# Kernel optimization log

Hardware: AMD Instinct MI355X
Metric: run time of the kernel (lower is better)

The kernel has to match this reference:

```python
import jax, jax.numpy as jnp
import numpy as np

B, S, D = 2, 2048, 1024
H = 16
HD = D // H  # 64

def setup_inputs() -> dict:
    key = jax.random.key(0)
    k1, k2, k3 = jax.random.split(key, 3)
    scale = 0.02
    return {
        "x": jax.random.normal(k1, (B, S, D), dtype=jnp.float32),
        "w_qkv": jax.random.normal(k2, (D, 3 * D), dtype=jnp.float32) * scale,
        "b_qkv": jnp.zeros((3 * D,), dtype=jnp.float32),
        "w_proj": jax.random.normal(k3, (D, D), dtype=jnp.float32) * scale,
        "b_proj": jnp.zeros((D,), dtype=jnp.float32),
    }

def reference(x, w_qkv, b_qkv, w_proj, b_proj):
    batch, seq_len, _ = x.shape
    qkv = x @ w_qkv + b_qkv                      # [B,S,3D]
    qkv = qkv.reshape(batch, seq_len, 3, H, HD)
    qkv = jnp.transpose(qkv, (2, 0, 3, 1, 4))    # [3,B,H,S,HD]
    q, k, v = qkv[0], qkv[1], qkv[2]
    attn = jnp.einsum('bhqd,bhkd->bhqk', q, k) / jnp.sqrt(jnp.float32(HD))
    attn = jax.nn.softmax(attn, axis=-1)         # [B,H,S,S]
    out = jnp.einsum('bhqk,bhkd->bhqd', attn, v)
    out = jnp.transpose(out, (0, 2, 1, 3)).reshape(batch, seq_len, -1)
    return out @ w_proj + b_proj
```

## Files before the change

### kernel.cpp

```cpp
#include <hip/hip_runtime.h>
#include <math.h>

#define SS 2048
#define DD 1024
#define HH 16
#define NQKV 3072
#define MROWS 4096
#define KD 1024

typedef __attribute__((ext_vector_type(8))) short bf16x8;
typedef __attribute__((ext_vector_type(8))) unsigned short us8;
typedef __attribute__((ext_vector_type(4))) float f32x4;
typedef unsigned short u16;
typedef unsigned int u32;

#define SCALE_C 0.18033688011112042f

#define GLDS16(g, l) \
  __builtin_amdgcn_global_load_lds((const __attribute__((address_space(1))) u32*)(g), \
                                   (__attribute__((address_space(3))) u32*)(l), 16, 0, 0)

static __device__ __forceinline__ u16 f2bf(float f) {
  union { float f; u32 u; } v; v.f = f;
  u32 u = v.u;
  u += 0x7fffu + ((u >> 16) & 1u);
  return (u16)(u >> 16);
}
static __device__ __forceinline__ u32 pk2(float a, float b) {
  return (u32)f2bf(a) | ((u32)f2bf(b) << 16);
}
static __device__ __forceinline__ u32 pk2t(float a, float b) {
  union { float f; u32 u; } ua, ub; ua.f = a; ub.f = b;
  return __builtin_amdgcn_perm(ub.u, ua.u, 0x07060302u);
}

__global__ __launch_bounds__(256) void k_prep(const float* __restrict__ x,
                                              const float* __restrict__ w_qkv,
                                              const float* __restrict__ w_proj,
                                              u16* __restrict__ x_bf,
                                              u16* __restrict__ wqkvT,
                                              u16* __restrict__ wprojT) {
  __shared__ float t[64][65];
  int bx = blockIdx.x;
  int tid = threadIdx.x;
  if (bx < 2048) {
    int i = (bx * 256 + tid) * 8;
    float4 a = *(const float4*)(x + i);
    float4 b = *(const float4*)(x + i + 4);
    us8 o;
    o[0] = f2bf(a.x); o[1] = f2bf(a.y); o[2] = f2bf(a.z); o[3] = f2bf(a.w);
    o[4] = f2bf(b.x); o[5] = f2bf(b.y); o[6] = f2bf(b.z); o[7] = f2bf(b.w);
    *(us8*)(x_bf + i) = o;
    return;
  }
  const float* in; u16* out; int R = KD, C, tile;
  if (bx < 2048 + 768) { in = w_qkv; out = wqkvT; C = NQKV; tile = bx - 2048; }
  else                 { in = w_proj; out = wprojT; C = DD; tile = bx - 2816; }
  int tilesC = C >> 6;
  int tc = tile % tilesC, tr = tile / tilesC;
  int r0 = tr * 64, c0 = tc * 64;
  int lx = tid & 63, ly = tid >> 6;
#pragma unroll
  for (int i = 0; i < 16; i++) {
    int rr = ly + i * 4;
    t[rr][lx] = in[(size_t)(r0 + rr) * C + c0 + lx];
  }
  __syncthreads();
#pragma unroll
  for (int i = 0; i < 16; i++) {
    int cc = ly + i * 4;
    out[(size_t)(c0 + cc) * R + r0 + lx] = f2bf(t[lx][cc]);
  }
}

template <int MODE, int BM>
__global__ __launch_bounds__(256, 2) void k_gemm(const u16* __restrict__ A,
                                                 const u16* __restrict__ Bt,
                                                 const float* __restrict__ bias,
                                                 void* __restrict__ Cout,
                                                 u16* __restrict__ vt,
                                                 int M, int N, int K) {
  constexpr int MT = BM / 32;
  __shared__ alignas(16) u16 As[BM * 64];
  __shared__ alignas(16) u16 Bs[128 * 64];
  const int tid = threadIdx.x;
  const int w = tid >> 6, ln = tid & 63;
  const int wm = w >> 1, wn = w & 1;
  const int lm = ln & 15, quad = ln >> 4;
  const int m0 = blockIdx.y * BM, n0 = blockIdx.x * 128;
  const int lr = ln >> 3, cc = ln & 7;
  const int cg = cc ^ lr;

  f32x4 acc[MT][4];
#pragma unroll
  for (int i = 0; i < MT; i++)
#pragma unroll
    for (int j = 0; j < 4; j++) acc[i][j] = (f32x4){0.f, 0.f, 0.f, 0.f};

  const u16* gA = A  + (size_t)(m0 + lr) * K + cg * 8;
  const u16* gB = Bt + (size_t)(n0 + lr) * K + cg * 8;

  for (int k0 = 0; k0 < K; k0 += 64) {
#pragma unroll
    for (int ii = 0; ii < MT; ii++) {
      int i = w + 4 * ii;
      GLDS16(gA + (size_t)(8 * i) * K + k0, (char*)As + i * 1024);
    }
#pragma unroll
    for (int ii = 0; ii < 4; ii++) {
      int i = w + 4 * ii;
      GLDS16(gB + (size_t)(8 * i) * K + k0, (char*)Bs + i * 1024);
    }
    __syncthreads();
    bf16x8 af[MT][2], bfr[4][2];
#pragma unroll
    for (int t = 0; t < MT; t++)
#pragma unroll
      for (int kk = 0; kk < 2; kk++)
        af[t][kk] = *(const bf16x8*)((const char*)As + (wm * (MT * 16) + t * 16 + lm) * 128 +
                                     (((kk * 4 + quad) ^ (lm & 7)) * 16));
#pragma unroll
    for (int t = 0; t < 4; t++)
#pragma unroll
      for (int kk = 0; kk < 2; kk++)
        bfr[t][kk] = *(const bf16x8*)((const char*)Bs + (wn * 64 + t * 16 + lm) * 128 +
                                      (((kk * 4 + quad) ^ (lm & 7)) * 16));
#pragma unroll
    for (int kk = 0; kk < 2; kk++)
#pragma unroll
      for (int mt = 0; mt < MT; mt++)
#pragma unroll
        for (int nt = 0; nt < 4; nt++)
          acc[mt][nt] = __builtin_amdgcn_mfma_f32_16x16x32_bf16(af[mt][kk], bfr[nt][kk], acc[mt][nt], 0, 0, 0);
    __syncthreads();
  }

  float bv[4];
#pragma unroll
  for (int nt = 0; nt < 4; nt++) bv[nt] = bias[n0 + wn * 64 + nt * 16 + lm];

  if (MODE == 2 && n0 >= 2 * DD) {
    int b = m0 >> 11;
    int s0 = (m0 & 2047) + wm * 64;
#pragma unroll
    for (int mt = 0; mt < MT; mt++) {
      int s = s0 + mt * 16 + quad * 4;
#pragma unroll
      for (int nt = 0; nt < 4; nt++) {
        int n = n0 + wn * 64 + nt * 16 + lm;
        int bh = b * HH + ((n - 2 * DD) >> 6);
        int d = n & 63;
        uint2 v;
        v.x = pk2(acc[mt][nt][0] + bv[nt], acc[mt][nt][1] + bv[nt]);
        v.y = pk2(acc[mt][nt][2] + bv[nt], acc[mt][nt][3] + bv[nt]);
        *(uint2*)&vt[(size_t)(bh * 64 + d) * SS + s] = v;
      }
    }
    return;
  }

  const float qs = (MODE == 2 && n0 < DD) ? SCALE_C : 1.0f;
#pragma unroll
  for (int mt = 0; mt < MT; mt++) {
#pragma unroll
    for (int r = 0; r < 4; r++) {
      int row = m0 + wm * (MT * 16) + mt * 16 + quad * 4 + r;
#pragma unroll
      for (int nt = 0; nt < 4; nt++) {
        int col = n0 + wn * 64 + nt * 16 + lm;
        float v = (acc[mt][nt][r] + bv[nt]) * qs;
        if (MODE == 2) ((u16*)Cout)[(size_t)row * N + col] = f2bf(v);
        else           ((float*)Cout)[(size_t)row * N + col] = v;
      }
    }
  }
}

__global__ __launch_bounds__(256, 2) void k_attn(const u16* __restrict__ qkv,
                                                 const u16* __restrict__ vt,
                                                 u16* __restrict__ attn) {
  __shared__ alignas(16) u16 Ks[2][128 * 64];
  __shared__ alignas(16) u16 Vs[2][64 * 128];
  __shared__ alignas(16) u16 Ps[4 * 32 * 64];

  const int tid = threadIdx.x;
  const int w = tid >> 6, ln = tid & 63;
  const int lm = ln & 15, quad = ln >> 4;
  const int bx = blockIdx.x;
  const int bh = bx >> 4;
  const int q0 = (bx & 15) * 128;
  const int b = bh >> 4, h = bh & 15;
  const size_t qkv_b = (size_t)b * SS * NQKV;
  const int hcol = h * 64;

  const int lr = ln >> 3, cc = ln & 7;
  const int cg = cc ^ lr;
  const int vr = ln >> 4, c16 = ln & 15;

  bf16x8 qf[2][2];
#pragma unroll
  for (int qs2 = 0; qs2 < 2; qs2++)
#pragma unroll
    for (int kk = 0; kk < 2; kk++)
      qf[qs2][kk] = *(const bf16x8*)(qkv + qkv_b +
                     (size_t)(q0 + w * 32 + qs2 * 16 + lm) * NQKV + hcol + kk * 32 + quad * 8);

  f32x4 o[4][2];
  float l[2] = {0.f, 0.f};
#pragma unroll
  for (int t = 0; t < 4; t++) { o[t][0] = (f32x4){0, 0, 0, 0}; o[t][1] = (f32x4){0, 0, 0, 0}; }

  char* psw = (char*)Ps + w * 4096;

#pragma unroll
  for (int rr = 0; rr < 4; rr++) {
    int i = w + 4 * rr;
    GLDS16(qkv + qkv_b + (size_t)(8 * i + lr) * NQKV + DD + hcol + cg * 8, (char*)Ks[0] + i * 1024);
    int cgv = c16 ^ ((4 * i + vr) & 15);
    GLDS16(vt + (size_t)(bh * 64 + 4 * i + vr) * SS + cgv * 8,             (char*)Vs[0] + i * 1024);
  }

#pragma unroll 1
  for (int it = 0; it < SS / 128; it++) {
    __syncthreads();

    if (it + 1 < SS / 128) {
      int kv1 = (it + 1) * 128;
      char* kd = (char*)Ks[(it + 1) & 1];
      char* vd = (char*)Vs[(it + 1) & 1];
#pragma unroll
      for (int rr = 0; rr < 4; rr++) {
        int i = w + 4 * rr;
        GLDS16(qkv + qkv_b + (size_t)(kv1 + 8 * i + lr) * NQKV + DD + hcol + cg * 8, kd + i * 1024);
        int cgv = c16 ^ ((4 * i + vr) & 15);
        GLDS16(vt + (size_t)(bh * 64 + 4 * i + vr) * SS + kv1 + cgv * 8,             vd + i * 1024);
      }
    }

    const char* ksb = (const char*)Ks[it & 1];
    const char* vsb = (const char*)Vs[it & 1];

#pragma unroll
    for (int sub = 0; sub < 2; sub++) {
      f32x4 s[4][2];
#pragma unroll
      for (int t = 0; t < 4; t++) { s[t][0] = (f32x4){0, 0, 0, 0}; s[t][1] = (f32x4){0, 0, 0, 0}; }
#pragma unroll
      for (int kk = 0; kk < 2; kk++)
#pragma unroll
        for (int t = 0; t < 4; t++) {
          bf16x8 kf = *(const bf16x8*)(ksb + (sub * 64 + t * 16 + lm) * 128 +
                                       (((kk * 4 + quad) ^ (lm & 7)) * 16));
          s[t][0] = __builtin_amdgcn_mfma_f32_16x16x32_bf16(kf, qf[0][kk], s[t][0], 0, 0, 0);
          s[t][1] = __builtin_amdgcn_mfma_f32_16x16x32_bf16(kf, qf[1][kk], s[t][1], 0, 0, 0);
        }

      bf16x8 vf[2][4];
#pragma unroll
      for (int kk = 0; kk < 2; kk++)
#pragma unroll
        for (int t = 0; t < 4; t++)
          vf[kk][t] = *(const bf16x8*)(vsb + (t * 16 + lm) * 256 +
                                       (((sub * 8 + kk * 4 + quad) ^ lm) * 16));

#pragma unroll
      for (int qs2 = 0; qs2 < 2; qs2++) {
        float sum = 0.f;
        u32 pkv[4][2];
#pragma unroll
        for (int t = 0; t < 4; t++) {
          float p0 = __builtin_amdgcn_exp2f(s[t][qs2][0]);
          float p1 = __builtin_amdgcn_exp2f(s[t][qs2][1]);
          float p2 = __builtin_amdgcn_exp2f(s[t][qs2][2]);
          float p3 = __builtin_amdgcn_exp2f(s[t][qs2][3]);
          sum += (p0 + p1) + (p2 + p3);
          pkv[t][0] = pk2t(p0, p1);
          pkv[t][1] = pk2t(p2, p3);
        }
        sum += __shfl_xor(sum, 16);
        sum += __shfl_xor(sum, 32);
        l[qs2] += sum;
#pragma unroll
        for (int t = 0; t < 4; t++) {
          uint2 v; v.x = pkv[t][0]; v.y = pkv[t][1];
          *(uint2*)(psw + (qs2 * 16 + lm) * 128 +
                    (((2 * t + (quad >> 1)) ^ (lm & 7)) * 16) + (quad & 1) * 8) = v;
        }
      }

      bf16x8 pf[2][2];
#pragma unroll
      for (int qs2 = 0; qs2 < 2; qs2++)
#pragma unroll
        for (int kk = 0; kk < 2; kk++)
          pf[qs2][kk] = *(const bf16x8*)(psw + (qs2 * 16 + lm) * 128 +
                                         (((kk * 4 + quad) ^ (lm & 7)) * 16));
#pragma unroll
      for (int kk = 0; kk < 2; kk++)
#pragma unroll
        for (int t = 0; t < 4; t++) {
          o[t][0] = __builtin_amdgcn_mfma_f32_16x16x32_bf16(vf[kk][t], pf[0][kk], o[t][0], 0, 0, 0);
          o[t][1] = __builtin_amdgcn_mfma_f32_16x16x32_bf16(vf[kk][t], pf[1][kk], o[t][1], 0, 0, 0);
        }
    }
  }

#pragma unroll
  for (int qs2 = 0; qs2 < 2; qs2++) {
    float il = 1.0f / l[qs2];
    int row = b * SS + q0 + w * 32 + qs2 * 16 + lm;
#pragma unroll
    for (int t = 0; t < 4; t++) {
      uint2 v;
      v.x = pk2(o[t][qs2][0] * il, o[t][qs2][1] * il);
      v.y = pk2(o[t][qs2][2] * il, o[t][qs2][3] * il);
      *(uint2*)&attn[(size_t)row * DD + hcol + t * 16 + quad * 4] = v;
    }
  }
}

extern "C" void kernel_launch(void* const* d_in, const int* in_sizes, int n_in,
                              void* d_out, int out_size, void* d_ws, size_t ws_size,
                              hipStream_t stream) {
  const float* x      = (const float*)d_in[0];
  const float* w_qkv  = (const float*)d_in[1];
  const float* b_qkv  = (const float*)d_in[2];
  const float* w_proj = (const float*)d_in[3];
  const float* b_proj = (const float*)d_in[4];
  float* out = (float*)d_out;

  u16* ws     = (u16*)d_ws;
  u16* x_bf   = ws;
  u16* wqkvT  = x_bf   + (size_t)MROWS * KD;
  u16* wprojT = wqkvT  + (size_t)NQKV * KD;
  u16* qkv    = wprojT + (size_t)DD * KD;
  u16* attn   = qkv    + (size_t)MROWS * NQKV;
  u16* vt     = attn   + (size_t)MROWS * DD;

  k_prep<<<3072, 256, 0, stream>>>(x, w_qkv, w_proj, x_bf, wqkvT, wprojT);
  k_gemm<2, 128><<<dim3(NQKV / 128, MROWS / 128), 256, 0, stream>>>(x_bf, wqkvT, b_qkv, qkv, vt, MROWS, NQKV, KD);
  k_attn<<<2 * HH * (SS / 128), 256, 0, stream>>>(qkv, vt, attn);
  k_gemm<0, 64><<<dim3(DD / 128, MROWS / 64), 256, 0, stream>>>(attn, wprojT, b_proj, out, nullptr, MROWS, DD, KD);
}
```

Baseline: 177.0 us.

## Switch attention kernel to 32x32x16 bf16 MFMA tiles

Rewrites the attention inner loop to use 32x32x16 MFMA instructions in place of 16x16x32. Each wave now handles 32 query rows as one tile, and the per-sub-block row sum needs a single cross-half shuffle at the end instead of two shuffles per step. The aim is fewer MFMA issues and fewer LDS fragment loads per unit of work. The price is new fragment layouts for K, V and P that must line up with the swizzled LDS layout, plus larger accumulators that raise register pressure.

```diff
diff --git a/kernel.cpp b/kernel.cpp
--- a/kernel.cpp
+++ b/kernel.cpp
@@ -11,6 +11,7 @@
 typedef __attribute__((ext_vector_type(8))) short bf16x8;
 typedef __attribute__((ext_vector_type(8))) unsigned short us8;
 typedef __attribute__((ext_vector_type(4))) float f32x4;
+typedef __attribute__((ext_vector_type(16))) float f32x16;
 typedef unsigned short u16;
 typedef unsigned int u32;
 
@@ -185,7 +186,7 @@
 
   const int tid = threadIdx.x;
   const int w = tid >> 6, ln = tid & 63;
-  const int lm = ln & 15, quad = ln >> 4;
+  const int qn = ln & 31, h5 = ln >> 5;
   const int bx = blockIdx.x;
   const int bh = bx >> 4;
   const int q0 = (bx & 15) * 128;
@@ -197,18 +198,17 @@
   const int cg = cc ^ lr;
   const int vr = ln >> 4, c16 = ln & 15;
 
-  bf16x8 qf[2][2];
-#pragma unroll
-  for (int qs2 = 0; qs2 < 2; qs2++)
-#pragma unroll
-    for (int kk = 0; kk < 2; kk++)
-      qf[qs2][kk] = *(const bf16x8*)(qkv + qkv_b +
-                     (size_t)(q0 + w * 32 + qs2 * 16 + lm) * NQKV + hcol + kk * 32 + quad * 8);
-
-  f32x4 o[4][2];
-  float l[2] = {0.f, 0.f};
-#pragma unroll
-  for (int t = 0; t < 4; t++) { o[t][0] = (f32x4){0, 0, 0, 0}; o[t][1] = (f32x4){0, 0, 0, 0}; }
+  bf16x8 qf[4];
+  {
+    const u16* qp = qkv + qkv_b + (size_t)(q0 + w * 32 + qn) * NQKV + hcol + h5 * 8;
+#pragma unroll
+    for (int ks = 0; ks < 4; ks++) qf[ks] = *(const bf16x8*)(qp + ks * 16);
+  }
+
+  f32x16 o[2];
+#pragma unroll
+  for (int i = 0; i < 16; i++) { o[0][i] = 0.f; o[1][i] = 0.f; }
+  float lsum = 0.f;
 
   char* psw = (char*)Ps + w * 4096;
 
@@ -242,81 +242,75 @@
 
 #pragma unroll
     for (int sub = 0; sub < 2; sub++) {
-      f32x4 s[4][2];
-#pragma unroll
-      for (int t = 0; t < 4; t++) { s[t][0] = (f32x4){0, 0, 0, 0}; s[t][1] = (f32x4){0, 0, 0, 0}; }
-#pragma unroll
-      for (int kk = 0; kk < 2; kk++)
-#pragma unroll
-        for (int t = 0; t < 4; t++) {
-          bf16x8 kf = *(const bf16x8*)(ksb + (sub * 64 + t * 16 + lm) * 128 +
-                                       (((kk * 4 + quad) ^ (lm & 7)) * 16));
-          s[t][0] = __builtin_amdgcn_mfma_f32_16x16x32_bf16(kf, qf[0][kk], s[t][0], 0, 0, 0);
-          s[t][1] = __builtin_amdgcn_mfma_f32_16x16x32_bf16(kf, qf[1][kk], s[t][1], 0, 0, 0);
+      f32x16 s0, s1;
+#pragma unroll
+      for (int i = 0; i < 16; i++) { s0[i] = 0.f; s1[i] = 0.f; }
+#pragma unroll
+      for (int ks = 0; ks < 4; ks++) {
+        int ch = 2 * ks + h5;
+        bf16x8 kf0 = *(const bf16x8*)(ksb + (sub * 64 + qn) * 128 + ((ch ^ (qn & 7)) * 16));
+        bf16x8 kf1 = *(const bf16x8*)(ksb + (sub * 64 + 32 + qn) * 128 + ((ch ^ (qn & 7)) * 16));
+        s0 = __builtin_amdgcn_mfma_f32_32x32x16_bf16(kf0, qf[ks], s0, 0, 0, 0);
+        s1 = __builtin_amdgcn_mfma_f32_32x32x16_bf16(kf1, qf[ks], s1, 0, 0, 0);
+      }
+
+      bf16x8 vf[2][4];
+#pragma unroll
+      for (int dm = 0; dm < 2; dm++)
+#pragma unroll
+        for (int ks2 = 0; ks2 < 4; ks2++) {
+          int d = dm * 32 + qn;
+          int ch16 = 8 * sub + 2 * ks2 + h5;
+          vf[dm][ks2] = *(const bf16x8*)(vsb + d * 256 + ((ch16 ^ (qn & 15)) * 16));
         }
 
-      bf16x8 vf[2][4];
-#pragma unroll
-      for (int kk = 0; kk < 2; kk++)
-#pragma unroll
-        for (int t = 0; t < 4; t++)
-          vf[kk][t] = *(const bf16x8*)(vsb + (t * 16 + lm) * 256 +
-                                       (((sub * 8 + kk * 4 + quad) ^ lm) * 16));
-
-#pragma unroll
-      for (int qs2 = 0; qs2 < 2; qs2++) {
-        float sum = 0.f;
-        u32 pkv[4][2];
-#pragma unroll
-        for (int t = 0; t < 4; t++) {
-          float p0 = __builtin_amdgcn_exp2f(s[t][qs2][0]);
-          float p1 = __builtin_amdgcn_exp2f(s[t][qs2][1]);
-          float p2 = __builtin_amdgcn_exp2f(s[t][qs2][2]);
-          float p3 = __builtin_amdgcn_exp2f(s[t][qs2][3]);
-          sum += (p0 + p1) + (p2 + p3);
-          pkv[t][0] = pk2t(p0, p1);
-          pkv[t][1] = pk2t(p2, p3);
-        }
-        sum += __shfl_xor(sum, 16);
-        sum += __shfl_xor(sum, 32);
-        l[qs2] += sum;
-#pragma unroll
-        for (int t = 0; t < 4; t++) {
-          uint2 v; v.x = pkv[t][0]; v.y = pkv[t][1];
-          *(uint2*)(psw + (qs2 * 16 + lm) * 128 +
-                    (((2 * t + (quad >> 1)) ^ (lm & 7)) * 16) + (quad & 1) * 8) = v;
-        }
-      }
-
-      bf16x8 pf[2][2];
-#pragma unroll
-      for (int qs2 = 0; qs2 < 2; qs2++)
-#pragma unroll
-        for (int kk = 0; kk < 2; kk++)
-          pf[qs2][kk] = *(const bf16x8*)(psw + (qs2 * 16 + lm) * 128 +
-                                         (((kk * 4 + quad) ^ (lm & 7)) * 16));
-#pragma unroll
-      for (int kk = 0; kk < 2; kk++)
-#pragma unroll
-        for (int t = 0; t < 4; t++) {
-          o[t][0] = __builtin_amdgcn_mfma_f32_16x16x32_bf16(vf[kk][t], pf[0][kk], o[t][0], 0, 0, 0);
-          o[t][1] = __builtin_amdgcn_mfma_f32_16x16x32_bf16(vf[kk][t], pf[1][kk], o[t][1], 0, 0, 0);
-        }
-    }
-  }
-
-#pragma unroll
-  for (int qs2 = 0; qs2 < 2; qs2++) {
-    float il = 1.0f / l[qs2];
-    int row = b * SS + q0 + w * 32 + qs2 * 16 + lm;
-#pragma unroll
-    for (int t = 0; t < 4; t++) {
+      float p0[16], p1[16];
+      float sum = 0.f;
+#pragma unroll
+      for (int r = 0; r < 16; r++) {
+        p0[r] = __builtin_amdgcn_exp2f(s0[r]);
+        p1[r] = __builtin_amdgcn_exp2f(s1[r]);
+        sum += p0[r] + p1[r];
+      }
+      lsum += sum;
+
+#pragma unroll
+      for (int g = 0; g < 4; g++) {
+        uint2 v0, v1;
+        v0.x = pk2t(p0[4 * g], p0[4 * g + 1]);
+        v0.y = pk2t(p0[4 * g + 2], p0[4 * g + 3]);
+        v1.x = pk2t(p1[4 * g], p1[4 * g + 1]);
+        v1.y = pk2t(p1[4 * g + 2], p1[4 * g + 3]);
+        *(uint2*)(psw + qn * 128 + ((g ^ (qn & 7)) * 16) + h5 * 8) = v0;
+        *(uint2*)(psw + qn * 128 + (((4 + g) ^ (qn & 7)) * 16) + h5 * 8) = v1;
+      }
+
+      bf16x8 pf[4];
+#pragma unroll
+      for (int ks2 = 0; ks2 < 4; ks2++)
+        pf[ks2] = *(const bf16x8*)(psw + qn * 128 + (((2 * ks2 + h5) ^ (qn & 7)) * 16));
+
+#pragma unroll
+      for (int ks2 = 0; ks2 < 4; ks2++) {
+        o[0] = __builtin_amdgcn_mfma_f32_32x32x16_bf16(vf[0][ks2], pf[ks2], o[0], 0, 0, 0);
+        o[1] = __builtin_amdgcn_mfma_f32_32x32x16_bf16(vf[1][ks2], pf[ks2], o[1], 0, 0, 0);
+      }
+    }
+  }
+
+  lsum += __shfl_xor(lsum, 32);
+  float il = 1.0f / lsum;
+  int row = b * SS + q0 + w * 32 + qn;
+#pragma unroll
+  for (int dm = 0; dm < 2; dm++)
+#pragma unroll
+    for (int g = 0; g < 4; g++) {
+      int d = dm * 32 + 8 * g + 4 * h5;
       uint2 v;
-      v.x = pk2(o[t][qs2][0] * il, o[t][qs2][1] * il);
-      v.y = pk2(o[t][qs2][2] * il, o[t][qs2][3] * il);
-      *(uint2*)&attn[(size_t)row * DD + hcol + t * 16 + quad * 4] = v;
-    }
-  }
+      v.x = pk2(o[dm][4 * g] * il, o[dm][4 * g + 1] * il);
+      v.y = pk2(o[dm][4 * g + 2] * il, o[dm][4 * g + 3] * il);
+      *(uint2*)&attn[(size_t)row * DD + hcol + d] = v;
+    }
 }
 
 extern "C" void kernel_launch(void* const* d_in, const int* in_sizes, int n_in,
```

Result: no change. 176.4 us (-0.3%).
